# Optimization experiments

Measured on AMD Instinct MI355X. Metric: run time of the kernel, lower is better.

## Reference

```python
import jax, jax.numpy as jnp
import numpy as np

EPS_LA = 1e-8
BN_EPS = 1e-5


def setup_inputs() -> dict:
    N, IN_C, HID, OUT_C = 8192, 64, 64, 32
    key = jax.random.key(0)
    ks = jax.random.split(key, 8)
    X = jax.random.normal(ks[0], (N, IN_C), dtype=jnp.float32)
    La = jax.random.uniform(ks[1], (N,), dtype=jnp.float32)  # eigenvalues in [0,1)
    U = jax.random.normal(ks[2], (N, N), dtype=jnp.float32)  # eigenvector matrix
    # learnable params
    ve = jnp.array([7.0], dtype=jnp.float32)   # Velocity(7)
    ve2 = jnp.array([0.0], dtype=jnp.float32)  # Velocity(0)
    W_w = jax.random.normal(ks[3], (HID, IN_C), dtype=jnp.float32) / np.sqrt(IN_C)
    W_b = jnp.zeros((HID,), dtype=jnp.float32)
    bn_gamma = jnp.ones((HID,), dtype=jnp.float32)
    bn_beta = jnp.zeros((HID,), dtype=jnp.float32)
    mlp_w = jax.random.normal(ks[4], (OUT_C, HID), dtype=jnp.float32) / np.sqrt(HID)
    mlp_b = jnp.zeros((OUT_C,), dtype=jnp.float32)
    return {"X": X, "La": La, "U": U, "ve": ve, "ve2": ve2,
            "W_w": W_w, "W_b": W_b, "bn_gamma": bn_gamma, "bn_beta": bn_beta,
            "mlp_w": mlp_w, "mlp_b": mlp_b}


def reference(X, La, U, ve, ve2, W_w, W_b, bn_gamma, bn_beta, mlp_w, mlp_b):
    # Spectral filter eigenvalue scalings (Velocity modules: elementwise pow)
    V_La = jnp.power(La, ve[0])                                # [N]
    V_La2 = jnp.power((2.0 * (La - EPS_LA) - 1.0) ** 2 + 1.0, ve2[0])  # [N]
    # U @ diag(V) @ U^T @ X done as elementwise scaling in the spectral domain
    # (same math as the dense diag-matmul chain, O(N^2 d) instead of O(N^3))
    out = U @ (V_La[:, None] * (U.T @ X))    # [N, in_c]
    out = U @ (V_La2[:, None] * (U.T @ out)) # [N, in_c]
    # Linear W
    out = out @ W_w.T + W_b                  # [N, hid]
    hidden_emd = out
    # BatchNorm1d (training-mode batch statistics, biased variance)
    mean = jnp.mean(out, axis=0)
    var = jnp.mean((out - mean) ** 2, axis=0)
    out = (out - mean) * jax.lax.rsqrt(var + BN_EPS) * bn_gamma + bn_beta
    # ReLU; dropout is identity in deterministic/eval reference
    out = jax.nn.relu(out)
    out = out @ mlp_w.T + mlp_b              # [N, out_c]
    return (jax.nn.log_softmax(out, axis=1), hidden_emd)
```

## Files before the change

kernel.cpp:

```cpp
#include <hip/hip_runtime.h>
#include <hip/hip_bf16.h>

typedef __attribute__((ext_vector_type(4))) float f32x4;
typedef __attribute__((ext_vector_type(8))) short bf16x8;
typedef __attribute__((ext_vector_type(8))) unsigned short u16x8;

#define NN 8192
#define SK 8
#define KSL (NN / SK)
#define NC (KSL / 64)

__device__ __forceinline__ unsigned short f2bf(float f) {
    unsigned int u = __float_as_uint(f);
    u += 0x7fffu + ((u >> 16) & 1u);
    return (unsigned short)(u >> 16);
}

__global__ __launch_bounds__(256) void prep_v(const float* __restrict__ La,
        const float* __restrict__ ve, const float* __restrict__ ve2,
        float* __restrict__ V1, float* __restrict__ V2) {
    int i = blockIdx.x * 256 + threadIdx.x;
    float la = La[i];
    V1[i] = powf(la, ve[0]);
    float b = 2.0f * (la - 1e-8f) - 1.0f;
    V2[i] = powf(b * b + 1.0f, ve2[0]);
}

template<int TRANS>
__global__ __launch_bounds__(256, 4) void gemm_pass(const float* __restrict__ U,
        const unsigned short* __restrict__ FB, float* __restrict__ P) {
    __shared__ float lds[4 * 1152];
    const int tid = threadIdx.x;
    const int w = tid >> 6, l = tid & 63;
    const int lm = l & 15, g = l >> 4;
    const int i0 = blockIdx.x * 64;
    const int kbase = blockIdx.y * KSL;
    const int m0 = i0 + w * 16;

    float* wlds = lds + w * 1152;

    const float* gbase = TRANS
        ? U + (size_t)(kbase + (l >> 2)) * NN + m0 + (l & 3) * 4
        : U + (size_t)(m0 + (l >> 2)) * NN + kbase + (l & 3) * 16;
    float* wptr = TRANS ? (wlds + 4 * l) : (wlds + (l >> 2) * 68 + (l & 3) * 16);

    const unsigned short* fbb =
        FB + ((size_t)(blockIdx.y * (KSL / 32)) * 4 * 64 + l) * 8;

    f32x4 acc[4];
#pragma unroll
    for (int nf = 0; nf < 4; ++nf) acc[nf] = (f32x4)0.f;

    f32x4 ra0[4], ra1[4];

#define ISSUE_A(r, c)                                                          \
    do {                                                                       \
        if (TRANS) {                                                           \
            const float* p_ = gbase + (size_t)(64 * (c)) * NN;                 \
            r[0] = *(const f32x4*)(p_);                                        \
            r[1] = *(const f32x4*)(p_ + (size_t)16 * NN);                      \
            r[2] = *(const f32x4*)(p_ + (size_t)32 * NN);                      \
            r[3] = *(const f32x4*)(p_ + (size_t)48 * NN);                      \
        } else {                                                               \
            const float* p_ = gbase + 64 * (c);                                \
            r[0] = *(const f32x4*)(p_);                                        \
            r[1] = *(const f32x4*)(p_ + 4);                                    \
            r[2] = *(const f32x4*)(p_ + 8);                                    \
            r[3] = *(const f32x4*)(p_ + 12);                                   \
        }                                                                      \
    } while (0)

#define ISSUE_B(bf, c)                                                         \
    do {                                                                       \
        _Pragma("unroll")                                                      \
        for (int sp_ = 0; sp_ < 2; ++sp_)                                      \
            _Pragma("unroll")                                                  \
            for (int nf_ = 0; nf_ < 4; ++nf_)                                  \
                bf[sp_ * 4 + nf_] = *(const bf16x8*)(fbb +                     \
                    (size_t)((2 * (c) + sp_) * 4 + nf_) * 512);                \
    } while (0)

#define DSW(r)                                                                 \
    do {                                                                       \
        if (TRANS) {                                                           \
            *(f32x4*)(wptr + 0)   = r[0];                                      \
            *(f32x4*)(wptr + 256) = r[1];                                      \
            *(f32x4*)(wptr + 512) = r[2];                                      \
            *(f32x4*)(wptr + 768) = r[3];                                      \
        } else {                                                               \
            *(f32x4*)(wptr + 0)  = r[0];                                       \
            *(f32x4*)(wptr + 4)  = r[1];                                       \
            *(f32x4*)(wptr + 8)  = r[2];                                       \
            *(f32x4*)(wptr + 12) = r[3];                                       \
        }                                                                      \
    } while (0)

#define COMP(bf)                                                               \
    do {                                                                       \
        _Pragma("unroll")                                                      \
        for (int sp_ = 0; sp_ < 2; ++sp_) {                                    \
            bf16x8 afr_;                                                       \
            if (TRANS) {                                                       \
                const float* rp_ = wlds + (32 * sp_ + 8 * g) * 16 + lm;        \
                _Pragma("unroll")                                              \
                for (int j_ = 0; j_ < 8; ++j_)                                 \
                    afr_[j_] = (short)f2bf(rp_[j_ * 16]);                      \
            } else {                                                           \
                const float* rp_ = wlds + lm * 68 + 32 * sp_ + 8 * g;          \
                f32x4 a0_ = *(const f32x4*)rp_;                                \
                f32x4 a1_ = *(const f32x4*)(rp_ + 4);                          \
                _Pragma("unroll")                                              \
                for (int j_ = 0; j_ < 4; ++j_) {                               \
                    afr_[j_]     = (short)f2bf(a0_[j_]);                       \
                    afr_[4 + j_] = (short)f2bf(a1_[j_]);                       \
                }                                                              \
            }                                                                  \
            _Pragma("unroll")                                                  \
            for (int nf_ = 0; nf_ < 4; ++nf_)                                  \
                acc[nf_] = __builtin_amdgcn_mfma_f32_16x16x32_bf16(            \
                    afr_, bf[sp_ * 4 + nf_], acc[nf_], 0, 0, 0);               \
        }                                                                      \
    } while (0)

    ISSUE_A(ra0, 0);
#pragma unroll
    for (int c = 0; c < NC; c += 2) {
        {
            bf16x8 bf[8];
            ISSUE_B(bf, c);
            if (c + 1 < NC) ISSUE_A(ra1, c + 1);
            DSW(ra0);
            COMP(bf);
        }
        {
            bf16x8 bf[8];
            ISSUE_B(bf, c + 1);
            if (c + 2 < NC) ISSUE_A(ra0, c + 2);
            DSW(ra1);
            COMP(bf);
        }
    }
#undef ISSUE_A
#undef ISSUE_B
#undef DSW
#undef COMP

    float* Pp = P + (size_t)blockIdx.y * NN * 64;
#pragma unroll
    for (int nf = 0; nf < 4; ++nf)
#pragma unroll
        for (int r = 0; r < 4; ++r)
            Pp[(size_t)(m0 + 4 * g + r) * 64 + nf * 16 + lm] = acc[nf][r];
}

__global__ __launch_bounds__(256) void reduce_t(const float* __restrict__ M, int nsk,
        const float* __restrict__ V, unsigned short* __restrict__ FB) {
    __shared__ float T[32][65];
    int b = blockIdx.x;
    int i0 = b * 32;
    int tid = threadIdx.x;
    int il = tid >> 3, jq = (tid & 7) * 8;
    f32x4 s0 = (f32x4)0.f, s1 = (f32x4)0.f;
    for (int k = 0; k < nsk; ++k) {
        const float* p = M + ((size_t)k * NN + i0 + il) * 64 + jq;
        s0 += *(const f32x4*)p;
        s1 += *(const f32x4*)(p + 4);
    }
    float sc = V ? V[i0 + il] : 1.0f;
#pragma unroll
    for (int c = 0; c < 4; ++c) {
        T[il][jq + c] = s0[c] * sc;
        T[il][jq + 4 + c] = s1[c] * sc;
    }
    __syncthreads();
    int nf = tid >> 6, l = tid & 63, g = l >> 4, lm = l & 15;
    u16x8 o;
#pragma unroll
    for (int s = 0; s < 8; ++s) o[s] = f2bf(T[8 * g + s][16 * nf + lm]);
    *(u16x8*)(FB + ((size_t)(b * 4 + nf) * 64 + l) * 8) = o;
}

__global__ __launch_bounds__(256) void reduce_linear(const float* __restrict__ P,
        const float* __restrict__ Ww, const float* __restrict__ Wb,
        float* __restrict__ hidden, float* __restrict__ bsum, float* __restrict__ bsq) {
    __shared__ float z[32][65];
    __shared__ float w[64][65];
    __shared__ float hl[32][65];
    int i0 = blockIdx.x * 32;
    int tid = threadIdx.x;
    for (int e = tid * 4; e < 4096; e += 1024) {
        f32x4 v = *(const f32x4*)(Ww + e);
        int h = e >> 6, c = e & 63;
#pragma unroll
        for (int q = 0; q < 4; ++q) w[h][c + q] = v[q];
    }
    int r = tid >> 3, c8 = (tid & 7) * 8;
    f32x4 a0 = (f32x4)0.f, a1 = (f32x4)0.f;
    for (int k = 0; k < SK; ++k) {
        const float* p = P + ((size_t)k * NN + i0 + r) * 64 + c8;
        a0 += *(const f32x4*)p;
        a1 += *(const f32x4*)(p + 4);
    }
#pragma unroll
    for (int q = 0; q < 4; ++q) { z[r][c8 + q] = a0[q]; z[r][c8 + 4 + q] = a1[q]; }
    __syncthreads();
    int h8 = (tid & 7) * 8;
#pragma unroll
    for (int hh = 0; hh < 8; ++hh) {
        int h = h8 + hh;
        float s = Wb[h];
        for (int c = 0; c < 64; ++c) s += z[r][c] * w[h][c];
        hidden[(size_t)(i0 + r) * 64 + h] = s;
        hl[r][h] = s;
    }
    __syncthreads();
    if (tid < 64) {
        float s = 0.f, q2 = 0.f;
#pragma unroll
        for (int rr = 0; rr < 32; ++rr) {
            float v = hl[rr][tid];
            s += v; q2 += v * v;
        }
        bsum[blockIdx.x * 64 + tid] = s;
        bsq[blockIdx.x * 64 + tid] = q2;
    }
}

__global__ __launch_bounds__(64) void bn_stats(const float* __restrict__ bsum,
        const float* __restrict__ bsq, const float* __restrict__ gamma,
        const float* __restrict__ beta, float* __restrict__ bnc) {
    int h = threadIdx.x;
    float s = 0.f, q = 0.f;
    for (int b = 0; b < 256; ++b) { s += bsum[b * 64 + h]; q += bsq[b * 64 + h]; }
    float mean = s / 8192.0f;
    float var = q / 8192.0f - mean * mean;
    float inv = rsqrtf(var + 1e-5f);
    float sc = gamma[h] * inv;
    bnc[h] = sc;
    bnc[64 + h] = beta[h] - mean * sc;
}

__global__ __launch_bounds__(256) void head(const float* __restrict__ hidden,
        const float* __restrict__ bnc, const float* __restrict__ Mw,
        const float* __restrict__ Mb, float* __restrict__ out0) {
    __shared__ float a[32][65];
    __shared__ float w[32][65];
    __shared__ float o[32][33];
    __shared__ float rowm[32];
    int i0 = blockIdx.x * 32;
    int tid = threadIdx.x;
    for (int e = tid * 4; e < 2048; e += 1024) {
        f32x4 v = *(const f32x4*)(Mw + e);
        int oo = e >> 6, c = e & 63;
#pragma unroll
        for (int q = 0; q < 4; ++q) w[oo][c + q] = v[q];
    }
    int r = tid >> 3, h8 = (tid & 7) * 8;
    const float* hp = hidden + (size_t)(i0 + r) * 64 + h8;
#pragma unroll
    for (int q = 0; q < 8; ++q) {
        int h = h8 + q;
        float v = hp[q] * bnc[h] + bnc[64 + h];
        a[r][h] = fmaxf(v, 0.f);
    }
    __syncthreads();
    int o4 = (tid & 7) * 4;
#pragma unroll
    for (int q = 0; q < 4; ++q) {
        int oo = o4 + q;
        float s = Mb[oo];
        for (int c = 0; c < 64; ++c) s += a[r][c] * w[oo][c];
        o[r][oo] = s;
    }
    __syncthreads();
    if (tid < 32) {
        float m = -3.0e38f;
#pragma unroll
        for (int c = 0; c < 32; ++c) m = fmaxf(m, o[tid][c]);
        float se = 0.f;
#pragma unroll
        for (int c = 0; c < 32; ++c) se += expf(o[tid][c] - m);
        rowm[tid] = m + logf(se);
    }
    __syncthreads();
    f32x4 v;
#pragma unroll
    for (int q = 0; q < 4; ++q) v[q] = o[r][o4 + q] - rowm[r];
    *(f32x4*)(out0 + (size_t)(i0 + r) * 32 + o4) = v;
}

extern "C" void kernel_launch(void* const* d_in, const int* in_sizes, int n_in,
                              void* d_out, int out_size, void* d_ws, size_t ws_size,
                              hipStream_t stream) {
    const float* X   = (const float*)d_in[0];
    const float* La  = (const float*)d_in[1];
    const float* U   = (const float*)d_in[2];
    const float* ve  = (const float*)d_in[3];
    const float* ve2 = (const float*)d_in[4];
    const float* Ww  = (const float*)d_in[5];
    const float* Wb  = (const float*)d_in[6];
    const float* gam = (const float*)d_in[7];
    const float* bet = (const float*)d_in[8];
    const float* Mw  = (const float*)d_in[9];
    const float* Mb  = (const float*)d_in[10];
    float* out0 = (float*)d_out;
    float* hidden = (float*)d_out + (size_t)NN * 32;

    char* ws = (char*)d_ws;
    float* V1   = (float*)ws;
    float* V2   = (float*)(ws + 32768);
    float* bsum = (float*)(ws + 65536);
    float* bsq  = (float*)(ws + 131072);
    float* bnc  = (float*)(ws + 196608);
    unsigned short* FB = (unsigned short*)(ws + 262144);
    float* P    = (float*)(ws + (2u << 20));

    prep_v<<<32, 256, 0, stream>>>(La, ve, ve2, V1, V2);
    reduce_t<<<256, 256, 0, stream>>>(X, 1, nullptr, FB);
    gemm_pass<1><<<dim3(NN / 64, SK), 256, 0, stream>>>(U, FB, P);
    reduce_t<<<256, 256, 0, stream>>>(P, SK, V1, FB);
    gemm_pass<0><<<dim3(NN / 64, SK), 256, 0, stream>>>(U, FB, P);
    reduce_t<<<256, 256, 0, stream>>>(P, SK, nullptr, FB);
    gemm_pass<1><<<dim3(NN / 64, SK), 256, 0, stream>>>(U, FB, P);
    reduce_t<<<256, 256, 0, stream>>>(P, SK, V2, FB);
    gemm_pass<0><<<dim3(NN / 64, SK), 256, 0, stream>>>(U, FB, P);
    reduce_linear<<<256, 256, 0, stream>>>(P, Ww, Wb, hidden, bsum, bsq);
    bn_stats<<<1, 64, 0, stream>>>(bsum, bsq, gam, bet, bnc);
    head<<<256, 256, 0, stream>>>(hidden, bnc, Mw, Mb, out0);
}
```

Baseline: 293.0 us.

## Drop LDS staging in GEMM passes; load MFMA fragments directly from global

Splits the templated GEMM into separate normal and transposed kernels. Both now load the U operand straight from global memory into registers in the layout the MFMA fragment expects, so the per-wave LDS write and read-back is gone. The transposed kernel swaps operand roles, with FB as the A operand and U columns as the B operand, and writes its partials transposed into a new Pt buffer. A new reduce2 kernel sums Pt across the K-slices, applies V, and packs to bf16 without LDS. The transposed path now does scalar strided loads of one float per row (16 loads per chunk), which may coalesce worse than the earlier float4 row loads.

New measurement: 307.6 us. 1.05x slower.

```diff
diff --git a/kernel.cpp b/kernel.cpp
--- a/kernel.cpp
+++ b/kernel.cpp
@@ -26,94 +26,50 @@
     V2[i] = powf(b * b + 1.0f, ve2[0]);
 }
 
-template<int TRANS>
-__global__ __launch_bounds__(256, 4) void gemm_pass(const float* __restrict__ U,
+
+__global__ __launch_bounds__(256, 4) void gemm_n(const float* __restrict__ U,
         const unsigned short* __restrict__ FB, float* __restrict__ P) {
-    __shared__ float lds[4 * 1152];
     const int tid = threadIdx.x;
     const int w = tid >> 6, l = tid & 63;
     const int lm = l & 15, g = l >> 4;
     const int i0 = blockIdx.x * 64;
     const int kbase = blockIdx.y * KSL;
+    const int kb0 = kbase >> 5;
     const int m0 = i0 + w * 16;
-
-    float* wlds = lds + w * 1152;
-
-    const float* gbase = TRANS
-        ? U + (size_t)(kbase + (l >> 2)) * NN + m0 + (l & 3) * 4
-        : U + (size_t)(m0 + (l >> 2)) * NN + kbase + (l & 3) * 16;
-    float* wptr = TRANS ? (wlds + 4 * l) : (wlds + (l >> 2) * 68 + (l & 3) * 16);
-
-    const unsigned short* fbb =
-        FB + ((size_t)(blockIdx.y * (KSL / 32)) * 4 * 64 + l) * 8;
+    const float* ap = U + (size_t)(m0 + lm) * NN + kbase + 8 * g;
+    const unsigned short* fbL = FB + (size_t)l * 8;
 
     f32x4 acc[4];
 #pragma unroll
     for (int nf = 0; nf < 4; ++nf) acc[nf] = (f32x4)0.f;
-
-    f32x4 ra0[4], ra1[4];
-
-#define ISSUE_A(r, c)                                                          \
-    do {                                                                       \
-        if (TRANS) {                                                           \
-            const float* p_ = gbase + (size_t)(64 * (c)) * NN;                 \
-            r[0] = *(const f32x4*)(p_);                                        \
-            r[1] = *(const f32x4*)(p_ + (size_t)16 * NN);                      \
-            r[2] = *(const f32x4*)(p_ + (size_t)32 * NN);                      \
-            r[3] = *(const f32x4*)(p_ + (size_t)48 * NN);                      \
-        } else {                                                               \
-            const float* p_ = gbase + 64 * (c);                                \
-            r[0] = *(const f32x4*)(p_);                                        \
-            r[1] = *(const f32x4*)(p_ + 4);                                    \
-            r[2] = *(const f32x4*)(p_ + 8);                                    \
-            r[3] = *(const f32x4*)(p_ + 12);                                   \
-        }                                                                      \
-    } while (0)
-
-#define ISSUE_B(bf, c)                                                         \
+    f32x4 a0[4], a1[4];
+
+#define NA(r, c)                                                               \
+    do {                                                                       \
+        const float* p_ = ap + 64 * (c);                                       \
+        r[0] = *(const f32x4*)(p_);                                            \
+        r[1] = *(const f32x4*)(p_ + 4);                                        \
+        r[2] = *(const f32x4*)(p_ + 32);                                       \
+        r[3] = *(const f32x4*)(p_ + 36);                                       \
+    } while (0)
+#define NB(bf, c)                                                              \
     do {                                                                       \
         _Pragma("unroll")                                                      \
         for (int sp_ = 0; sp_ < 2; ++sp_)                                      \
             _Pragma("unroll")                                                  \
             for (int nf_ = 0; nf_ < 4; ++nf_)                                  \
-                bf[sp_ * 4 + nf_] = *(const bf16x8*)(fbb +                     \
-                    (size_t)((2 * (c) + sp_) * 4 + nf_) * 512);                \
-    } while (0)
-
-#define DSW(r)                                                                 \
-    do {                                                                       \
-        if (TRANS) {                                                           \
-            *(f32x4*)(wptr + 0)   = r[0];                                      \
-            *(f32x4*)(wptr + 256) = r[1];                                      \
-            *(f32x4*)(wptr + 512) = r[2];                                      \
-            *(f32x4*)(wptr + 768) = r[3];                                      \
-        } else {                                                               \
-            *(f32x4*)(wptr + 0)  = r[0];                                       \
-            *(f32x4*)(wptr + 4)  = r[1];                                       \
-            *(f32x4*)(wptr + 8)  = r[2];                                       \
-            *(f32x4*)(wptr + 12) = r[3];                                       \
-        }                                                                      \
-    } while (0)
-
-#define COMP(bf)                                                               \
+                bf[sp_ * 4 + nf_] = *(const bf16x8*)(fbL +                     \
+                    ((size_t)((kb0 + 2 * (c) + sp_) * 4 + nf_)) * 512);        \
+    } while (0)
+#define NCOMP(r, bf)                                                           \
     do {                                                                       \
         _Pragma("unroll")                                                      \
         for (int sp_ = 0; sp_ < 2; ++sp_) {                                    \
             bf16x8 afr_;                                                       \
-            if (TRANS) {                                                       \
-                const float* rp_ = wlds + (32 * sp_ + 8 * g) * 16 + lm;        \
-                _Pragma("unroll")                                              \
-                for (int j_ = 0; j_ < 8; ++j_)                                 \
-                    afr_[j_] = (short)f2bf(rp_[j_ * 16]);                      \
-            } else {                                                           \
-                const float* rp_ = wlds + lm * 68 + 32 * sp_ + 8 * g;          \
-                f32x4 a0_ = *(const f32x4*)rp_;                                \
-                f32x4 a1_ = *(const f32x4*)(rp_ + 4);                          \
-                _Pragma("unroll")                                              \
-                for (int j_ = 0; j_ < 4; ++j_) {                               \
-                    afr_[j_]     = (short)f2bf(a0_[j_]);                       \
-                    afr_[4 + j_] = (short)f2bf(a1_[j_]);                       \
-                }                                                              \
+            _Pragma("unroll")                                                  \
+            for (int j_ = 0; j_ < 4; ++j_) {                                   \
+                afr_[j_]     = (short)f2bf(r[2 * sp_][j_]);                    \
+                afr_[4 + j_] = (short)f2bf(r[2 * sp_ + 1][j_]);                \
             }                                                                  \
             _Pragma("unroll")                                                  \
             for (int nf_ = 0; nf_ < 4; ++nf_)                                  \
@@ -122,29 +78,25 @@
         }                                                                      \
     } while (0)
 
-    ISSUE_A(ra0, 0);
+    NA(a0, 0);
 #pragma unroll
     for (int c = 0; c < NC; c += 2) {
         {
             bf16x8 bf[8];
-            ISSUE_B(bf, c);
-            if (c + 1 < NC) ISSUE_A(ra1, c + 1);
-            DSW(ra0);
-            COMP(bf);
+            NB(bf, c);
+            NA(a1, c + 1);
+            NCOMP(a0, bf);
         }
         {
             bf16x8 bf[8];
-            ISSUE_B(bf, c + 1);
-            if (c + 2 < NC) ISSUE_A(ra0, c + 2);
-            DSW(ra1);
-            COMP(bf);
-        }
-    }
-#undef ISSUE_A
-#undef ISSUE_B
-#undef DSW
-#undef COMP
-
+            NB(bf, c + 1);
+            if (c + 2 < NC) NA(a0, c + 2);
+            NCOMP(a1, bf);
+        }
+    }
+#undef NA
+#undef NB
+#undef NCOMP
     float* Pp = P + (size_t)blockIdx.y * NN * 64;
 #pragma unroll
     for (int nf = 0; nf < 4; ++nf)
@@ -153,8 +105,115 @@
             Pp[(size_t)(m0 + 4 * g + r) * 64 + nf * 16 + lm] = acc[nf][r];
 }
 
+__global__ __launch_bounds__(256, 4) void gemm_t(const float* __restrict__ U,
+        const unsigned short* __restrict__ FB, float* __restrict__ Pt) {
+    const int tid = threadIdx.x;
+    const int w = tid >> 6, l = tid & 63;
+    const int lm = l & 15, g = l >> 4;
+    const int i0 = blockIdx.x * 64;
+    const int col = i0 + 16 * w + lm;
+    const int kbase = blockIdx.y * KSL;
+    const int kb0 = kbase >> 5;
+    const float* up = U + (size_t)(kbase + 8 * g) * NN + col;
+    const unsigned short* fbL = FB + (size_t)l * 8;
+
+    f32x4 acc[4];
+#pragma unroll
+    for (int mf = 0; mf < 4; ++mf) acc[mf] = (f32x4)0.f;
+    float b0[16], b1[16];
+
+#define TB(br, c)                                                              \
+    do {                                                                       \
+        _Pragma("unroll")                                                      \
+        for (int sp_ = 0; sp_ < 2; ++sp_)                                      \
+            _Pragma("unroll")                                                  \
+            for (int s_ = 0; s_ < 8; ++s_)                                     \
+                br[sp_ * 8 + s_] =                                             \
+                    up[(size_t)((c) * 64 + sp_ * 32 + s_) * NN];               \
+    } while (0)
+#define TA(af, c)                                                              \
+    do {                                                                       \
+        _Pragma("unroll")                                                      \
+        for (int sp_ = 0; sp_ < 2; ++sp_)                                      \
+            _Pragma("unroll")                                                  \
+            for (int mf_ = 0; mf_ < 4; ++mf_)                                  \
+                af[sp_ * 4 + mf_] = *(const bf16x8*)(fbL +                     \
+                    ((size_t)((kb0 + 2 * (c) + sp_) * 4 + mf_)) * 512);        \
+    } while (0)
+#define TCOMP(af, br)                                                          \
+    do {                                                                       \
+        _Pragma("unroll")                                                      \
+        for (int sp_ = 0; sp_ < 2; ++sp_) {                                    \
+            bf16x8 bfr_;                                                       \
+            _Pragma("unroll")                                                  \
+            for (int s_ = 0; s_ < 8; ++s_)                                     \
+                bfr_[s_] = (short)f2bf(br[sp_ * 8 + s_]);                      \
+            _Pragma("unroll")                                                  \
+            for (int mf_ = 0; mf_ < 4; ++mf_)                                  \
+                acc[mf_] = __builtin_amdgcn_mfma_f32_16x16x32_bf16(            \
+                    af[sp_ * 4 + mf_], bfr_, acc[mf_], 0, 0, 0);               \
+        }                                                                      \
+    } while (0)
+
+    TB(b0, 0);
+#pragma unroll
+    for (int c = 0; c < NC; c += 2) {
+        {
+            bf16x8 af[8];
+            TB(b1, c + 1);
+            TA(af, c);
+            TCOMP(af, b0);
+        }
+        {
+            bf16x8 af[8];
+            if (c + 2 < NC) TB(b0, c + 2);
+            TA(af, c + 1);
+            TCOMP(af, b1);
+        }
+    }
+#undef TB
+#undef TA
+#undef TCOMP
+    float* Pp = Pt + (size_t)blockIdx.y * 64 * NN;
+#pragma unroll
+    for (int mf = 0; mf < 4; ++mf)
+#pragma unroll
+        for (int r = 0; r < 4; ++r)
+            Pp[(size_t)(mf * 16 + 4 * g + r) * NN + col] = acc[mf][r];
+}
+
+__global__ __launch_bounds__(256) void reduce2(const float* __restrict__ Pt,
+        const float* __restrict__ V, unsigned short* __restrict__ FB) {
+    int b = blockIdx.x;
+    int t = threadIdx.x;
+    int nf = t >> 6, l = t & 63, lm = l & 15, g = l >> 4;
+    int ch = 16 * nf + lm;
+    int ib = 32 * b + 8 * g;
+    f32x4 s0 = (f32x4)0.f, s1 = (f32x4)0.f;
+#pragma unroll
+    for (int sk = 0; sk < SK; ++sk) {
+        const float* p = Pt + (size_t)(sk * 64 + ch) * NN + ib;
+        s0 += *(const f32x4*)p;
+        s1 += *(const f32x4*)(p + 4);
+    }
+    f32x4 v0, v1;
+    if (V) {
+        v0 = *(const f32x4*)(V + ib);
+        v1 = *(const f32x4*)(V + ib + 4);
+    } else {
+        v0 = (f32x4)1.f; v1 = (f32x4)1.f;
+    }
+    u16x8 o;
+#pragma unroll
+    for (int c = 0; c < 4; ++c) {
+        o[c]     = f2bf(s0[c] * v0[c]);
+        o[4 + c] = f2bf(s1[c] * v1[c]);
+    }
+    *(u16x8*)(FB + ((size_t)(b * 4 + nf) * 64 + l) * 8) = o;
+}
+
 __global__ __launch_bounds__(256) void reduce_t(const float* __restrict__ M, int nsk,
-        const float* __restrict__ V, unsigned short* __restrict__ FB) {
+        unsigned short* __restrict__ FB) {
     __shared__ float T[32][65];
     int b = blockIdx.x;
     int i0 = b * 32;
@@ -166,11 +225,10 @@
         s0 += *(const f32x4*)p;
         s1 += *(const f32x4*)(p + 4);
     }
-    float sc = V ? V[i0 + il] : 1.0f;
 #pragma unroll
     for (int c = 0; c < 4; ++c) {
-        T[il][jq + c] = s0[c] * sc;
-        T[il][jq + 4 + c] = s1[c] * sc;
+        T[il][jq + c] = s0[c];
+        T[il][jq + 4 + c] = s1[c];
     }
     __syncthreads();
     int nf = tid >> 6, l = tid & 63, g = l >> 4, lm = l & 15;
@@ -314,16 +372,17 @@
     float* bnc  = (float*)(ws + 196608);
     unsigned short* FB = (unsigned short*)(ws + 262144);
     float* P    = (float*)(ws + (2u << 20));
+    float* Pt   = (float*)(ws + (20u << 20));
 
     prep_v<<<32, 256, 0, stream>>>(La, ve, ve2, V1, V2);
-    reduce_t<<<256, 256, 0, stream>>>(X, 1, nullptr, FB);
-    gemm_pass<1><<<dim3(NN / 64, SK), 256, 0, stream>>>(U, FB, P);
-    reduce_t<<<256, 256, 0, stream>>>(P, SK, V1, FB);
-    gemm_pass<0><<<dim3(NN / 64, SK), 256, 0, stream>>>(U, FB, P);
-    reduce_t<<<256, 256, 0, stream>>>(P, SK, nullptr, FB);
-    gemm_pass<1><<<dim3(NN / 64, SK), 256, 0, stream>>>(U, FB, P);
-    reduce_t<<<256, 256, 0, stream>>>(P, SK, V2, FB);
-    gemm_pass<0><<<dim3(NN / 64, SK), 256, 0, stream>>>(U, FB, P);
+    reduce_t<<<256, 256, 0, stream>>>(X, 1, FB);
+    gemm_t<<<dim3(NN / 64, SK), 256, 0, stream>>>(U, FB, Pt);
+    reduce2<<<256, 256, 0, stream>>>(Pt, V1, FB);
+    gemm_n<<<dim3(NN / 64, SK), 256, 0, stream>>>(U, FB, P);
+    reduce_t<<<256, 256, 0, stream>>>(P, SK, FB);
+    gemm_t<<<dim3(NN / 64, SK), 256, 0, stream>>>(U, FB, Pt);
+    reduce2<<<256, 256, 0, stream>>>(Pt, V2, FB);
+    gemm_n<<<dim3(NN / 64, SK), 256, 0, stream>>>(U, FB, P);
     reduce_linear<<<256, 256, 0, stream>>>(P, Ww, Wb, hidden, bsum, bsq);
     bn_stats<<<1, 64, 0, stream>>>(bsum, bsq, gam, bet, bnc);
     head<<<256, 256, 0, stream>>>(hidden, bnc, Mw, Mb, out0);
```

## Pre-convert U to bf16 and transpose once, simplify GEMM to direct loads

Applied to the files above, without the earlier changes.

Adds a kernel that converts U to bf16 in both normal and transposed layouts, so all four GEMM passes read contiguous bf16 A fragments straight into MFMA operands without LDS staging or per-pass conversion. Split-K is raised from 8 to 16. This halves the bytes each GEMM pass reads, at the cost of an extra full pass over U plus writing 256MB of bf16 copies, and larger partial-sum buffers for the reductions.

Result: slower. 360.3 us (+23.0%).

```diff
diff --git a/kernel.cpp b/kernel.cpp
--- a/kernel.cpp
+++ b/kernel.cpp
@@ -6,7 +6,7 @@
 typedef __attribute__((ext_vector_type(8))) unsigned short u16x8;
 
 #define NN 8192
-#define SK 8
+#define SK 16
 #define KSL (NN / SK)
 #define NC (KSL / 64)
 
@@ -26,125 +26,97 @@
     V2[i] = powf(b * b + 1.0f, ve2[0]);
 }
 
-template<int TRANS>
-__global__ __launch_bounds__(256, 4) void gemm_pass(const float* __restrict__ U,
+__global__ __launch_bounds__(256) void convert_u(const float* __restrict__ U,
+        unsigned short* __restrict__ Ubf, unsigned short* __restrict__ Utbf) {
+    __shared__ unsigned short t[64][72];
+    int i0 = blockIdx.y * 64, j0 = blockIdx.x * 64;
+    int tid = threadIdx.x;
+    int r = tid >> 3, c8 = (tid & 7) * 8;
+#pragma unroll
+    for (int it = 0; it < 2; ++it) {
+        int row = it * 32 + r;
+        const float* p = U + (size_t)(i0 + row) * NN + j0 + c8;
+        f32x4 a = *(const f32x4*)p;
+        f32x4 b = *(const f32x4*)(p + 4);
+        u16x8 o;
+#pragma unroll
+        for (int q = 0; q < 4; ++q) { o[q] = f2bf(a[q]); o[4 + q] = f2bf(b[q]); }
+        *(u16x8*)(Ubf + (size_t)(i0 + row) * NN + j0 + c8) = o;
+#pragma unroll
+        for (int q = 0; q < 8; ++q) t[row][c8 + q] = o[q];
+    }
+    __syncthreads();
+#pragma unroll
+    for (int it = 0; it < 2; ++it) {
+        int row = it * 32 + r;
+        u16x8 o;
+#pragma unroll
+        for (int q = 0; q < 8; ++q) o[q] = t[c8 + q][row];
+        *(u16x8*)(Utbf + (size_t)(j0 + row) * NN + i0 + c8) = o;
+    }
+}
+
+__global__ __launch_bounds__(256, 6) void gemm_n(const unsigned short* __restrict__ Ab,
         const unsigned short* __restrict__ FB, float* __restrict__ P) {
-    __shared__ float lds[4 * 1152];
     const int tid = threadIdx.x;
     const int w = tid >> 6, l = tid & 63;
     const int lm = l & 15, g = l >> 4;
     const int i0 = blockIdx.x * 64;
     const int kbase = blockIdx.y * KSL;
+    const int kb0 = kbase >> 5;
     const int m0 = i0 + w * 16;
-
-    float* wlds = lds + w * 1152;
-
-    const float* gbase = TRANS
-        ? U + (size_t)(kbase + (l >> 2)) * NN + m0 + (l & 3) * 4
-        : U + (size_t)(m0 + (l >> 2)) * NN + kbase + (l & 3) * 16;
-    float* wptr = TRANS ? (wlds + 4 * l) : (wlds + (l >> 2) * 68 + (l & 3) * 16);
-
-    const unsigned short* fbb =
-        FB + ((size_t)(blockIdx.y * (KSL / 32)) * 4 * 64 + l) * 8;
+    const unsigned short* ap = Ab + (size_t)(m0 + lm) * NN + kbase + 8 * g;
+    const unsigned short* fbL = FB + (size_t)l * 8;
 
     f32x4 acc[4];
 #pragma unroll
     for (int nf = 0; nf < 4; ++nf) acc[nf] = (f32x4)0.f;
-
-    f32x4 ra0[4], ra1[4];
-
-#define ISSUE_A(r, c)                                                          \
+    bf16x8 a0[2], a1[2];
+
+#define NA(r, c)                                                               \
     do {                                                                       \
-        if (TRANS) {                                                           \
-            const float* p_ = gbase + (size_t)(64 * (c)) * NN;                 \
-            r[0] = *(const f32x4*)(p_);                                        \
-            r[1] = *(const f32x4*)(p_ + (size_t)16 * NN);                      \
-            r[2] = *(const f32x4*)(p_ + (size_t)32 * NN);                      \
-            r[3] = *(const f32x4*)(p_ + (size_t)48 * NN);                      \
-        } else {                                                               \
-            const float* p_ = gbase + 64 * (c);                                \
-            r[0] = *(const f32x4*)(p_);                                        \
-            r[1] = *(const f32x4*)(p_ + 4);                                    \
-            r[2] = *(const f32x4*)(p_ + 8);                                    \
-            r[3] = *(const f32x4*)(p_ + 12);                                   \
-        }                                                                      \
+        const unsigned short* p_ = ap + 64 * (c);                              \
+        r[0] = *(const bf16x8*)(p_);                                           \
+        r[1] = *(const bf16x8*)(p_ + 32);                                      \
     } while (0)
-
-#define ISSUE_B(bf, c)                                                         \
+#define NB(bf, c)                                                              \
     do {                                                                       \
         _Pragma("unroll")                                                      \
         for (int sp_ = 0; sp_ < 2; ++sp_)                                      \
             _Pragma("unroll")                                                  \
             for (int nf_ = 0; nf_ < 4; ++nf_)                                  \
-                bf[sp_ * 4 + nf_] = *(const bf16x8*)(fbb +                     \
-                    (size_t)((2 * (c) + sp_) * 4 + nf_) * 512);                \
+                bf[sp_ * 4 + nf_] = *(const bf16x8*)(fbL +                     \
+                    ((size_t)((kb0 + 2 * (c) + sp_) * 4 + nf_)) * 512);        \
     } while (0)
-
-#define DSW(r)                                                                 \
-    do {                                                                       \
-        if (TRANS) {                                                           \
-            *(f32x4*)(wptr + 0)   = r[0];                                      \
-            *(f32x4*)(wptr + 256) = r[1];                                      \
-            *(f32x4*)(wptr + 512) = r[2];                                      \
-            *(f32x4*)(wptr + 768) = r[3];                                      \
-        } else {                                                               \
-            *(f32x4*)(wptr + 0)  = r[0];                                       \
-            *(f32x4*)(wptr + 4)  = r[1];                                       \
-            *(f32x4*)(wptr + 8)  = r[2];                                       \
-            *(f32x4*)(wptr + 12) = r[3];                                       \
-        }                                                                      \
-    } while (0)
-
-#define COMP(bf)                                                               \
+#define NCOMP(r, bf)                                                           \
     do {                                                                       \
         _Pragma("unroll")                                                      \
-        for (int sp_ = 0; sp_ < 2; ++sp_) {                                    \
-            bf16x8 afr_;                                                       \
-            if (TRANS) {                                                       \
-                const float* rp_ = wlds + (32 * sp_ + 8 * g) * 16 + lm;        \
-                _Pragma("unroll")                                              \
-                for (int j_ = 0; j_ < 8; ++j_)                                 \
-                    afr_[j_] = (short)f2bf(rp_[j_ * 16]);                      \
-            } else {                                                           \
-                const float* rp_ = wlds + lm * 68 + 32 * sp_ + 8 * g;          \
-                f32x4 a0_ = *(const f32x4*)rp_;                                \
-                f32x4 a1_ = *(const f32x4*)(rp_ + 4);                          \
-                _Pragma("unroll")                                              \
-                for (int j_ = 0; j_ < 4; ++j_) {                               \
-                    afr_[j_]     = (short)f2bf(a0_[j_]);                       \
-                    afr_[4 + j_] = (short)f2bf(a1_[j_]);                       \
-                }                                                              \
-            }                                                                  \
+        for (int sp_ = 0; sp_ < 2; ++sp_)                                      \
             _Pragma("unroll")                                                  \
             for (int nf_ = 0; nf_ < 4; ++nf_)                                  \
                 acc[nf_] = __builtin_amdgcn_mfma_f32_16x16x32_bf16(            \
-                    afr_, bf[sp_ * 4 + nf_], acc[nf_], 0, 0, 0);               \
-        }                                                                      \
+                    r[sp_], bf[sp_ * 4 + nf_], acc[nf_], 0, 0, 0);             \
     } while (0)
 
-    ISSUE_A(ra0, 0);
+    NA(a0, 0);
 #pragma unroll
     for (int c = 0; c < NC; c += 2) {
         {
             bf16x8 bf[8];
-            ISSUE_B(bf, c);
-            if (c + 1 < NC) ISSUE_A(ra1, c + 1);
-            DSW(ra0);
-            COMP(bf);
+            NB(bf, c);
+            NA(a1, c + 1);
+            NCOMP(a0, bf);
         }
         {
             bf16x8 bf[8];
-            ISSUE_B(bf, c + 1);
-            if (c + 2 < NC) ISSUE_A(ra0, c + 2);
-            DSW(ra1);
-            COMP(bf);
+            NB(bf, c + 1);
+            if (c + 2 < NC) NA(a0, c + 2);
+            NCOMP(a1, bf);
         }
     }
-#undef ISSUE_A
-#undef ISSUE_B
-#undef DSW
-#undef COMP
-
+#undef NA
+#undef NB
+#undef NCOMP
     float* Pp = P + (size_t)blockIdx.y * NN * 64;
 #pragma unroll
     for (int nf = 0; nf < 4; ++nf)
@@ -314,16 +286,19 @@
     float* bnc  = (float*)(ws + 196608);
     unsigned short* FB = (unsigned short*)(ws + 262144);
     float* P    = (float*)(ws + (2u << 20));
+    unsigned short* Ubf  = (unsigned short*)(ws + (64u << 20));
+    unsigned short* Utbf = (unsigned short*)(ws + (192u << 20));
 
     prep_v<<<32, 256, 0, stream>>>(La, ve, ve2, V1, V2);
+    convert_u<<<dim3(128, 128), 256, 0, stream>>>(U, Ubf, Utbf);
     reduce_t<<<256, 256, 0, stream>>>(X, 1, nullptr, FB);
-    gemm_pass<1><<<dim3(NN / 64, SK), 256, 0, stream>>>(U, FB, P);
+    gemm_n<<<dim3(NN / 64, SK), 256, 0, stream>>>(Utbf, FB, P);
     reduce_t<<<256, 256, 0, stream>>>(P, SK, V1, FB);
-    gemm_pass<0><<<dim3(NN / 64, SK), 256, 0, stream>>>(U, FB, P);
+    gemm_n<<<dim3(NN / 64, SK), 256, 0, stream>>>(Ubf, FB, P);
     reduce_t<<<256, 256, 0, stream>>>(P, SK, nullptr, FB);
-    gemm_pass<1><<<dim3(NN / 64, SK), 256, 0, stream>>>(U, FB, P);
+    gemm_n<<<dim3(NN / 64, SK), 256, 0, stream>>>(Utbf, FB, P);
     reduce_t<<<256, 256, 0, stream>>>(P, SK, V2, FB);
-    gemm_pass<0><<<dim3(NN / 64, SK), 256, 0, stream>>>(U, FB, P);
+    gemm_n<<<dim3(NN / 64, SK), 256, 0, stream>>>(Ubf, FB, P);
     reduce_linear<<<256, 256, 0, stream>>>(P, Ww, Wb, hidden, bsum, bsq);
     bn_stats<<<1, 64, 0, stream>>>(bsum, bsq, gam, bet, bnc);
     head<<<256, 256, 0, stream>>>(hidden, bnc, Mw, Mb, out0);
```
